# Kernel optimization log

Hardware: AMD Instinct MI355X
Metric: run time of the kernel (lower is better)

The kernel has to match this reference:

```python
import jax, jax.numpy as jnp
import numpy as np

V, BLK, H, D, L = 32000, 1024, 16, 1024, 3
HD = D // H  # 64
B, T = 4, 1024


def _layernorm(x, g, b, eps=1e-5):
    mu = jnp.mean(x, axis=-1, keepdims=True)
    var = jnp.mean(jnp.square(x - mu), axis=-1, keepdims=True)
    return (x - mu) * jax.lax.rsqrt(var + eps) * g + b


def setup_inputs() -> dict:
    key = jax.random.key(0)
    ks = jax.random.split(key, 32)
    s = 0.02
    inp = {}
    inp["idx"] = jax.random.randint(ks[0], (B, T), 0, V)
    inp["target"] = jax.random.randint(ks[1], (B, T), 0, V)
    inp["tok_emb"] = jax.random.normal(ks[2], (V, D), jnp.float32) * s
    inp["pos_emb"] = jax.random.normal(ks[3], (BLK, D), jnp.float32) * s
    inp["wq"] = jax.random.normal(ks[4], (L, H, D, HD), jnp.float32) * s
    inp["wk"] = jax.random.normal(ks[5], (L, H, D, HD), jnp.float32) * s
    inp["wv"] = jax.random.normal(ks[6], (L, H, D, HD), jnp.float32) * s
    inp["wproj"] = jax.random.normal(ks[7], (L, D, D), jnp.float32) * s
    inp["bproj"] = jnp.zeros((L, D), jnp.float32)
    inp["ln1_g"] = jnp.ones((L, D), jnp.float32)
    inp["ln1_b"] = jnp.zeros((L, D), jnp.float32)
    inp["ln2_g"] = jnp.ones((L, D), jnp.float32)
    inp["ln2_b"] = jnp.zeros((L, D), jnp.float32)
    inp["w1"] = jax.random.normal(ks[8], (L, D, 4 * D), jnp.float32) * s
    inp["b1"] = jnp.zeros((L, 4 * D), jnp.float32)
    inp["w2"] = jax.random.normal(ks[9], (L, 4 * D, D), jnp.float32) * s
    inp["b2"] = jnp.zeros((L, D), jnp.float32)
    inp["lnf_g"] = jnp.ones((D,), jnp.float32)
    inp["lnf_b"] = jnp.zeros((D,), jnp.float32)
    inp["wlm"] = jax.random.normal(ks[10], (D, V), jnp.float32) * s
    inp["blm"] = jnp.zeros((V,), jnp.float32)
    return inp


def reference(idx, target, tok_emb, pos_emb, wq, wk, wv, wproj, bproj,
              ln1_g, ln1_b, ln2_g, ln2_b, w1, b1, w2, b2,
              lnf_g, lnf_b, wlm, blm):
    Bb, Tt = idx.shape
    x = tok_emb[idx] + pos_emb[:Tt]  # [B,T,D]
    mask = jnp.tril(jnp.ones((Tt, Tt), dtype=bool))  # causal
    scale = D ** -0.5  # NOTE: source scales by n_embd**-0.5, not head_size**-0.5
    for l in range(L):
        xn = _layernorm(x, ln1_g[l], ln1_b[l])
        q = jnp.einsum('btd,hde->bhte', xn, wq[l])
        k = jnp.einsum('btd,hde->bhte', xn, wk[l])
        v = jnp.einsum('btd,hde->bhte', xn, wv[l])
        scores = jnp.einsum('bhte,bhse->bhts', q, k) * scale
        scores = jnp.where(mask, scores, -jnp.inf)
        attn = jax.nn.softmax(scores, axis=-1)
        o = jnp.einsum('bhts,bhse->bhte', attn, v)
        o = o.transpose(0, 2, 1, 3).reshape(Bb, Tt, D)  # concat heads
        x = x + o @ wproj[l] + bproj[l]
        xn2 = _layernorm(x, ln2_g[l], ln2_b[l])
        h = jax.nn.relu(xn2 @ w1[l] + b1[l])
        x = x + h @ w2[l] + b2[l]
    x = _layernorm(x, lnf_g, lnf_b)
    logits = x @ wlm + blm  # [B,T,V]
    logp = jax.nn.log_softmax(logits, axis=-1)
    nll = -jnp.take_along_axis(logp, target[..., None], axis=-1)[..., 0]
    loss = jnp.mean(nll)
    return logits, loss
```

## Files before the change

### kernel.cpp

```cpp
#include <hip/hip_runtime.h>
#include <math.h>

#define Dn   1024
#define Hn   16
#define HDn  64
#define Tn   1024
#define Bn   4
#define Vn   32000
#define Ln   3
#define NT   (Bn*Tn)

typedef __attribute__((ext_vector_type(8))) short bf16x8;
typedef __attribute__((ext_vector_type(4))) float f32x4;

__device__ __forceinline__ float b2f(unsigned short u) {
  union { float f; unsigned int i; } c; c.i = ((unsigned int)u) << 16; return c.f;
}
__device__ __forceinline__ unsigned short f2b(float f) {
  union { float f; unsigned int i; } c; c.f = f;
  unsigned int r = (c.i + 0x7FFFu + ((c.i >> 16) & 1u)) >> 16;
  return (unsigned short)r;
}

#define GLOAD_LDS16(g, l) __builtin_amdgcn_global_load_lds( \
    (const __attribute__((address_space(1))) void*)(g),     \
    (__attribute__((address_space(3))) void*)(l), 16, 0, 0)

#define SBAR()  __builtin_amdgcn_s_barrier()
#define SCHED() __builtin_amdgcn_sched_barrier(0)

__global__ __launch_bounds__(256) void embed_kernel(
    const int* __restrict__ idx, const float* __restrict__ tok,
    const float* __restrict__ pos, float* __restrict__ x) {
  int row = blockIdx.x;
  int t = row & (Tn - 1);
  int token = idx[row];
  const float4* tp = (const float4*)(tok + (size_t)token * Dn);
  const float4* pp = (const float4*)(pos + (size_t)t * Dn);
  float4* xp = (float4*)(x + (size_t)row * Dn);
  int i = threadIdx.x;
  float4 a = tp[i], b = pp[i];
  xp[i] = make_float4(a.x + b.x, a.y + b.y, a.z + b.z, a.w + b.w);
}

__global__ __launch_bounds__(256) void ln_kernel(
    const float* __restrict__ x, const float* __restrict__ g,
    const float* __restrict__ b, unsigned short* __restrict__ y) {
  int row = blockIdx.x;
  const float4* xr = (const float4*)(x + (size_t)row * Dn);
  __shared__ float red[4];
  int lane = threadIdx.x & 63, w = threadIdx.x >> 6;

  float4 v = xr[threadIdx.x];
  float s = v.x + v.y + v.z + v.w;
  #pragma unroll
  for (int o = 32; o > 0; o >>= 1) s += __shfl_down(s, o, 64);
  if (lane == 0) red[w] = s;
  __syncthreads();
  float mu = (red[0] + red[1] + red[2] + red[3]) * (1.0f / Dn);
  __syncthreads();

  float dx = v.x - mu, dy = v.y - mu, dz = v.z - mu, dw = v.w - mu;
  float ss = dx*dx + dy*dy + dz*dz + dw*dw;
  #pragma unroll
  for (int o = 32; o > 0; o >>= 1) ss += __shfl_down(ss, o, 64);
  if (lane == 0) red[w] = ss;
  __syncthreads();
  float var = (red[0] + red[1] + red[2] + red[3]) * (1.0f / Dn);
  float inv = rsqrtf(var + 1e-5f);

  float4 gv = ((const float4*)g)[threadIdx.x];
  float4 bv = ((const float4*)b)[threadIdx.x];
  ushort4 o4;
  o4.x = f2b(dx*inv*gv.x + bv.x);
  o4.y = f2b(dy*inv*gv.y + bv.y);
  o4.z = f2b(dz*inv*gv.z + bv.z);
  o4.w = f2b(dw*inv*gv.w + bv.w);
  ((ushort4*)(y + (size_t)row * Dn))[threadIdx.x] = o4;
}

__global__ __launch_bounds__(256) void wcast_kernel(
    const float* __restrict__ src, unsigned short* __restrict__ dst,
    int K, int M, long long bsk, long long bsh) {
  __shared__ float t[32][33];
  int m0 = blockIdx.x << 5, k0 = blockIdx.y << 5;
  int tid = threadIdx.x;
  int ml = tid & 31, kl = tid >> 5;
  #pragma unroll
  for (int p = 0; p < 4; ++p) {
    int k = k0 + kl + p * 8;
    int m = m0 + ml;
    t[ml][kl + p * 8] = src[(size_t)k * bsk + (size_t)(m >> 6) * bsh + (m & 63)];
  }
  __syncthreads();
  int kl2 = tid & 31, ml2 = tid >> 5;
  #pragma unroll
  for (int p = 0; p < 4; ++p) {
    int m = m0 + ml2 + p * 8;
    int k = k0 + kl2;
    dst[(size_t)m * K + k] = f2b(t[ml2 + p * 8][kl2]);
  }
}

__global__ __launch_bounds__(256) void wcast3_kernel(
    const float* __restrict__ s0, const float* __restrict__ s1,
    const float* __restrict__ s2, unsigned short* __restrict__ dst) {
  const float* src = (blockIdx.z == 0) ? s0 : (blockIdx.z == 1) ? s1 : s2;
  unsigned short* d = dst + (size_t)blockIdx.z * 1024 * Dn;
  __shared__ float t[32][33];
  int m0 = blockIdx.x << 5, k0 = blockIdx.y << 5;
  int tid = threadIdx.x;
  int ml = tid & 31, kl = tid >> 5;
  #pragma unroll
  for (int p = 0; p < 4; ++p) {
    int k = k0 + kl + p * 8;
    int m = m0 + ml;
    t[ml][kl + p * 8] = src[(size_t)k * HDn + (size_t)(m >> 6) * (Dn * HDn) + (m & 63)];
  }
  __syncthreads();
  int kl2 = tid & 31, ml2 = tid >> 5;
  #pragma unroll
  for (int p = 0; p < 4; ++p) {
    int m = m0 + ml2 + p * 8;
    int k = k0 + kl2;
    d[(size_t)m * Dn + k] = f2b(t[ml2 + p * 8][kl2]);
  }
}

__global__ __launch_bounds__(512) void mm_bf16(
    const unsigned short* __restrict__ A, const unsigned short* __restrict__ BT,
    const float* __restrict__ bias, const float* __restrict__ res,
    float* __restrict__ Cf, unsigned short* __restrict__ Ch,
    int N, int K, int M, int relu) {
  __shared__ __align__(16) unsigned short As[3][128 * 32];
  __shared__ __align__(16) unsigned short Bs[3][128 * 32];
  const int tid = threadIdx.x;
  const int lane = tid & 63, w = tid >> 6, g = lane >> 4;
  const int wr = w >> 2, wc = w & 3;
  const int n0 = blockIdx.x << 7, m0 = blockIdx.y << 7;

  f32x4 acc[4][2];
  #pragma unroll
  for (int i = 0; i < 4; ++i)
    #pragma unroll
    for (int j = 0; j < 2; ++j)
      acc[i][j] = (f32x4){0.f, 0.f, 0.f, 0.f};

  const int srow = tid >> 2, su = tid & 3;
  const int sks = su ^ ((srow >> 1) & 3);
  const unsigned short* a_g = A + (size_t)(n0 + srow) * K + sks * 8;
  const unsigned short* b_g = BT + (size_t)(m0 + srow) * K + sks * 8;

  int a_off[4], b_off[2];
  #pragma unroll
  for (int f = 0; f < 4; ++f) {
    int row = wr * 64 + f * 16 + (lane & 15);
    a_off[f] = row * 64 + ((g ^ ((row >> 1) & 3)) << 4);
  }
  #pragma unroll
  for (int f = 0; f < 2; ++f) {
    int col = wc * 32 + f * 16 + (lane & 15);
    b_off[f] = col * 64 + ((g ^ ((col >> 1) & 3)) << 4);
  }

#define MM_STAGE(buf, kk) do {                                   \
    GLOAD_LDS16(a_g + (kk), As[buf] + tid * 8);                  \
    GLOAD_LDS16(b_g + (kk), Bs[buf] + tid * 8); } while (0)

#define MM_COMPUTE(buf) do {                                     \
    bf16x8 af[4], bfr[2];                                        \
    _Pragma("unroll")                                            \
    for (int f = 0; f < 4; ++f)                                  \
      af[f] = *(const bf16x8*)((const char*)As[buf] + a_off[f]); \
    _Pragma("unroll")                                            \
    for (int f = 0; f < 2; ++f)                                  \
      bfr[f] = *(const bf16x8*)((const char*)Bs[buf] + b_off[f]);\
    _Pragma("unroll")                                            \
    for (int i = 0; i < 4; ++i)                                  \
      _Pragma("unroll")                                          \
      for (int j = 0; j < 2; ++j)                                \
        acc[i][j] = __builtin_amdgcn_mfma_f32_16x16x32_bf16(af[i], bfr[j], acc[i][j], 0, 0, 0); } while (0)

  MM_STAGE(0, 0);
  MM_STAGE(1, 32);
  int bc = 0, bp = 2;
  for (int k0 = 0; k0 < K; k0 += 32) {
    if (k0 + 32 < K) asm volatile("s_waitcnt vmcnt(2)" ::: "memory");
    else             asm volatile("s_waitcnt vmcnt(0)" ::: "memory");
    SCHED(); SBAR(); SCHED();
    if (k0 + 64 < K) MM_STAGE(bp, k0 + 64);
    MM_COMPUTE(bc);
    bc = (bc == 2) ? 0 : bc + 1;
    bp = (bp == 2) ? 0 : bp + 1;
  }

  #pragma unroll
  for (int fc = 0; fc < 2; ++fc) {
    int colg = m0 + wc * 32 + fc * 16 + (lane & 15);
    float bz = bias ? bias[colg] : 0.f;
    #pragma unroll
    for (int fr = 0; fr < 4; ++fr) {
      #pragma unroll
      for (int i = 0; i < 4; ++i) {
        int rowg = n0 + wr * 64 + fr * 16 + (g << 2) + i;
        float v = acc[fr][fc][i] + bz;
        if (res) v += res[(size_t)rowg * M + colg];
        if (relu) v = fmaxf(v, 0.f);
        if (Cf) Cf[(size_t)rowg * M + colg] = v;
        else    Ch[(size_t)rowg * M + colg] = f2b(v);
      }
    }
  }
#undef MM_STAGE
#undef MM_COMPUTE
}

template<int OMODE>
__global__ __launch_bounds__(512) void mm512_bf16(
    const unsigned short* __restrict__ A, const unsigned short* __restrict__ BT,
    const float* __restrict__ bias, const float* __restrict__ res,
    float* __restrict__ Cf, unsigned short* __restrict__ Ch,
    float* __restrict__ rowsum, int N, int K, int M, int relu) {
  __shared__ __align__(16) unsigned short As[3][128 * 32];
  __shared__ __align__(16) unsigned short Bs[3][256 * 32];
  __shared__ float rsum2[OMODE == 4 ? 128 * 4 : 4];
  const int tid = threadIdx.x;
  const int lane = tid & 63, w = tid >> 6, g = lane >> 4;
  const int wr = w >> 2, wc = w & 3;
  const int n0 = blockIdx.x << 7, m0 = blockIdx.y << 8;

  f32x4 acc[4][4];
  #pragma unroll
  for (int i = 0; i < 4; ++i)
    #pragma unroll
    for (int j = 0; j < 4; ++j)
      acc[i][j] = (f32x4){0.f, 0.f, 0.f, 0.f};

  const int arow = tid >> 2, au = tid & 3;
  const int aks = au ^ ((arow >> 1) & 3);
  const unsigned short* a_g = A + (size_t)(n0 + arow) * K + aks * 8;
  const int brow1 = (tid + 512) >> 2;
  const int bks0 = au ^ ((arow >> 1) & 3);
  const int bks1 = au ^ ((brow1 >> 1) & 3);
  const unsigned short* b_g0 = BT + (size_t)(m0 + arow) * K + bks0 * 8;
  const unsigned short* b_g1 = BT + (size_t)(m0 + brow1) * K + bks1 * 8;

  int a_off[4], b_off[4];
  #pragma unroll
  for (int f = 0; f < 4; ++f) {
    int row = wr * 64 + f * 16 + (lane & 15);
    a_off[f] = row * 64 + ((g ^ ((row >> 1) & 3)) << 4);
    int col = wc * 64 + f * 16 + (lane & 15);
    b_off[f] = col * 64 + ((g ^ ((col >> 1) & 3)) << 4);
  }

#define MM5_STAGE(buf, kk) do {                                  \
    GLOAD_LDS16(a_g + (kk), As[buf] + tid * 8);                  \
    GLOAD_LDS16(b_g0 + (kk), Bs[buf] + tid * 8);                 \
    GLOAD_LDS16(b_g1 + (kk), Bs[buf] + (tid + 512) * 8); } while (0)

#define MM5_COMPUTE(buf) do {                                    \
    bf16x8 af[4], bfr[4];                                        \
    _Pragma("unroll")                                            \
    for (int f = 0; f < 4; ++f) {                                \
      af[f]  = *(const bf16x8*)((const char*)As[buf] + a_off[f]);\
      bfr[f] = *(const bf16x8*)((const char*)Bs[buf] + b_off[f]);\
    }                                                            \
    _Pragma("unroll")                                            \
    for (int i = 0; i < 4; ++i)                                  \
      _Pragma("unroll")                                          \
      for (int j = 0; j < 4; ++j)                                \
        acc[i][j] = __builtin_amdgcn_mfma_f32_16x16x32_bf16(af[i], bfr[j], acc[i][j], 0, 0, 0); } while (0)

  MM5_STAGE(0, 0);
  MM5_STAGE(1, 32);
  int bc = 0, bp = 2;
  for (int k0 = 0; k0 < K; k0 += 32) {
    if (k0 + 32 < K) asm volatile("s_waitcnt vmcnt(3)" ::: "memory");
    else             asm volatile("s_waitcnt vmcnt(0)" ::: "memory");
    SCHED(); SBAR(); SCHED();
    if (k0 + 64 < K) MM5_STAGE(bp, k0 + 64);
    MM5_COMPUTE(bc);
    bc = (bc == 2) ? 0 : bc + 1;
    bp = (bp == 2) ? 0 : bp + 1;
  }

  if (OMODE == 0) {
    #pragma unroll
    for (int fc = 0; fc < 4; ++fc) {
      int colg = m0 + wc * 64 + fc * 16 + (lane & 15);
      float bz = bias ? bias[colg] : 0.f;
      #pragma unroll
      for (int fr = 0; fr < 4; ++fr) {
        #pragma unroll
        for (int i = 0; i < 4; ++i) {
          int rowg = n0 + wr * 64 + fr * 16 + (g << 2) + i;
          float v = acc[fr][fc][i] + bz;
          if (res) v += res[(size_t)rowg * M + colg];
          if (relu) v = fmaxf(v, 0.f);
          if (Cf) Cf[(size_t)rowg * M + colg] = v;
          else    Ch[(size_t)rowg * M + colg] = f2b(v);
        }
      }
    }
  } else if (OMODE == 3) {
    unsigned short* kb  = Ch + (size_t)NT * Dn;
    unsigned short* vtb = Ch + 2 * (size_t)NT * Dn;
    #pragma unroll
    for (int fc = 0; fc < 4; ++fc) {
      int colg = m0 + wc * 64 + fc * 16 + (lane & 15);
      int sel = colg >> 10, hh = (colg >> 6) & 15, e = colg & 63;
      #pragma unroll
      for (int fr = 0; fr < 4; ++fr) {
        int rowg0 = n0 + wr * 64 + fr * 16 + (g << 2);
        int b = rowg0 >> 10, t0 = rowg0 & 1023;
        if (sel == 2) {
          ushort4 pk;
          pk.x = f2b(acc[fr][fc][0]); pk.y = f2b(acc[fr][fc][1]);
          pk.z = f2b(acc[fr][fc][2]); pk.w = f2b(acc[fr][fc][3]);
          *(ushort4*)&vtb[(((size_t)(b * 16 + hh) * 64) + e) * 1024 + t0] = pk;
        } else {
          unsigned short* dst = (sel == 0) ? Ch : kb;
          #pragma unroll
          for (int i = 0; i < 4; ++i)
            dst[(((size_t)(b * 16 + hh) * 1024) + t0 + i) * 64 + e] = f2b(acc[fr][fc][i]);
        }
      }
    }
  } else {
    #pragma unroll
    for (int fr = 0; fr < 4; ++fr) {
      #pragma unroll
      for (int i = 0; i < 4; ++i) {
        int rloc = wr * 64 + fr * 16 + (g << 2) + i;
        int rowg = n0 + rloc;
        float es = 0.f;
        #pragma unroll
        for (int fc = 0; fc < 4; ++fc) {
          int colg = m0 + wc * 64 + fc * 16 + (lane & 15);
          float v = acc[fr][fc][i] + bias[colg];
          __builtin_nontemporal_store(v, &Cf[(size_t)rowg * M + colg]);
          es += __expf(v);
        }
        es += __shfl_xor(es, 1); es += __shfl_xor(es, 2);
        es += __shfl_xor(es, 4); es += __shfl_xor(es, 8);
        if ((lane & 15) == 0) rsum2[rloc * 4 + wc] = es;
      }
    }
    __syncthreads();
    if (tid < 128)
      atomicAdd(&rowsum[n0 + tid],
                rsum2[tid * 4 + 0] + rsum2[tid * 4 + 1] +
                rsum2[tid * 4 + 2] + rsum2[tid * 4 + 3]);
  }
#undef MM5_STAGE
#undef MM5_COMPUTE
}

__global__ __launch_bounds__(256) void fattn_kernel(
    const unsigned short* __restrict__ qg, const unsigned short* __restrict__ kg,
    const unsigned short* __restrict__ vtg, unsigned short* __restrict__ ob) {
  const int bid = blockIdx.x;
  const int qt = bid & 15, bh = bid >> 4;
  const int b = bh >> 4, h = bh & 15;
  const int tid = threadIdx.x, lane = tid & 63, w = tid >> 6, g = lane >> 4;

  __shared__ __align__(16) unsigned short Ks[2][64 * 64];
  __shared__ __align__(16) unsigned short Vs[2][64 * 64];
  __shared__ __align__(16) unsigned short Pb[4][16 * 64];

  const unsigned short* kbase = kg + (size_t)bh * Tn * HDn;
  const unsigned short* vbase = vtg + (size_t)bh * HDn * Tn;

  const int qrow = qt * 64 + w * 16 + (lane & 15);
  const unsigned short* qptr = qg + ((size_t)bh * Tn + qrow) * HDn;
  bf16x8 qf0 = *(const bf16x8*)(qptr + g * 8);
  bf16x8 qf1 = *(const bf16x8*)(qptr + 32 + g * 8);

  f32x4 accO[4];
  #pragma unroll
  for (int dt = 0; dt < 4; ++dt) accO[dt] = (f32x4){0.f, 0.f, 0.f, 0.f};
  float mrun[4] = {-1e30f, -1e30f, -1e30f, -1e30f};
  float lrun[4] = {0.f, 0.f, 0.f, 0.f};

  const float scale = 0.03125f;
  const int qout0 = qt * 64 + w * 16 + 4 * g;

  unsigned short* pb = &Pb[w][0];
  const int nsteps = qt + 1;

#define FA_STAGE(buf, s0_) do {                                              \
    _Pragma("unroll")                                                        \
    for (int r = 0; r < 2; ++r) {                                            \
      int c = tid + 256 * r;                                                 \
      int srow = c >> 3, u = c & 7;                                          \
      GLOAD_LDS16(kbase + (size_t)((s0_) + srow) * HDn + ((u ^ (srow & 7)) * 8), Ks[buf] + c * 8); \
    }                                                                        \
    _Pragma("unroll")                                                        \
    for (int r = 0; r < 2; ++r) {                                            \
      int c = tid + 256 * r;                                                 \
      int d = c >> 3, u = c & 7;                                             \
      GLOAD_LDS16(vbase + (size_t)d * Tn + (s0_) + ((u ^ (d & 7)) * 8), Vs[buf] + c * 8); \
    } } while (0)

  FA_STAGE(0, 0);
  int cur = 0;

  for (int st = 0; st < nsteps; ++st) {
    const int s0 = st * 64;
    if (st + 1 < nsteps) {
      FA_STAGE(cur ^ 1, s0 + 64);
      asm volatile("s_waitcnt vmcnt(4)" ::: "memory");
    } else {
      asm volatile("s_waitcnt vmcnt(0)" ::: "memory");
    }
    SCHED(); SBAR(); SCHED();

    float p[4][4];
    #pragma unroll
    for (int sub = 0; sub < 4; ++sub) {
      int srow = sub * 16 + (lane & 15);
      const char* kr = (const char*)Ks[cur] + srow * 128;
      bf16x8 kf0 = *(const bf16x8*)(kr + ((g ^ (srow & 7)) * 16));
      bf16x8 kf1 = *(const bf16x8*)(kr + (((4 + g) ^ (srow & 7)) * 16));
      f32x4 s4 = (f32x4){0.f, 0.f, 0.f, 0.f};
      s4 = __builtin_amdgcn_mfma_f32_16x16x32_bf16(qf0, kf0, s4, 0, 0, 0);
      s4 = __builtin_amdgcn_mfma_f32_16x16x32_bf16(qf1, kf1, s4, 0, 0, 0);
      int sg = s0 + srow;
      #pragma unroll
      for (int i = 0; i < 4; ++i)
        p[sub][i] = (sg > qout0 + i) ? -1e30f : s4[i] * scale;
    }

    #pragma unroll
    for (int i = 0; i < 4; ++i) {
      float v = fmaxf(fmaxf(p[0][i], p[1][i]), fmaxf(p[2][i], p[3][i]));
      v = fmaxf(v, __shfl_xor(v, 1)); v = fmaxf(v, __shfl_xor(v, 2));
      v = fmaxf(v, __shfl_xor(v, 4)); v = fmaxf(v, __shfl_xor(v, 8));
      float nm = fmaxf(mrun[i], v);
      float fac = __expf(mrun[i] - nm);
      mrun[i] = nm;
      #pragma unroll
      for (int dt = 0; dt < 4; ++dt) accO[dt][i] *= fac;
      float sum = 0.f;
      #pragma unroll
      for (int sub = 0; sub < 4; ++sub) {
        float e = __expf(p[sub][i] - nm);
        p[sub][i] = e;
        sum += e;
      }
      sum += __shfl_xor(sum, 1); sum += __shfl_xor(sum, 2);
      sum += __shfl_xor(sum, 4); sum += __shfl_xor(sum, 8);
      lrun[i] = lrun[i] * fac + sum;
    }

    #pragma unroll
    for (int sub = 0; sub < 4; ++sub) {
      int s = sub * 16 + (lane & 15);
      #pragma unroll
      for (int i = 0; i < 4; ++i) {
        int q = 4 * g + i;
        pb[q * 64 + (((s >> 3) ^ (q & 7)) * 8) + (s & 7)] = f2b(p[sub][i]);
      }
    }

    #pragma unroll
    for (int sc = 0; sc < 2; ++sc) {
      int qq = lane & 15;
      bf16x8 pa = *(const bf16x8*)((const char*)pb + qq * 128 + (((sc * 4 + g) ^ (qq & 7)) * 16));
      #pragma unroll
      for (int dt = 0; dt < 4; ++dt) {
        int d = dt * 16 + (lane & 15);
        bf16x8 vf = *(const bf16x8*)((const char*)Vs[cur] + d * 128 + (((sc * 4 + g) ^ (d & 7)) * 16));
        accO[dt] = __builtin_amdgcn_mfma_f32_16x16x32_bf16(pa, vf, accO[dt], 0, 0, 0);
      }
    }

    SCHED(); SBAR(); SCHED();
    cur ^= 1;
  }
#undef FA_STAGE

  float rinv[4];
  #pragma unroll
  for (int i = 0; i < 4; ++i) rinv[i] = 1.0f / lrun[i];
  #pragma unroll
  for (int dt = 0; dt < 4; ++dt) {
    int dcol = h * 64 + dt * 16 + (lane & 15);
    #pragma unroll
    for (int i = 0; i < 4; ++i) {
      int t = qout0 + i;
      ob[((size_t)(b * Tn + t)) * Dn + dcol] = f2b(accO[dt][i] * rinv[i]);
    }
  }
}

__global__ __launch_bounds__(256) void loss_kernel(
    const float* __restrict__ logits, const float* __restrict__ rowsum,
    const int* __restrict__ target, float* __restrict__ out_loss) {
  __shared__ float red[4];
  int lane = threadIdx.x & 63, w = threadIdx.x >> 6;
  float s = 0.f;
  for (int row = threadIdx.x; row < NT; row += 256) {
    float lt = logits[(size_t)row * Vn + target[row]];
    s += logf(rowsum[row]) - lt;
  }
  #pragma unroll
  for (int off = 32; off > 0; off >>= 1) s += __shfl_down(s, off, 64);
  if (lane == 0) red[w] = s;
  __syncthreads();
  if (threadIdx.x == 0)
    *out_loss = (red[0] + red[1] + red[2] + red[3]) * (1.0f / NT);
}

static inline void launch_wcast(const float* src, unsigned short* dst, int K, int M,
                                long long bsk, long long bsh, hipStream_t s) {
  dim3 g(M >> 5, K >> 5);
  wcast_kernel<<<g, 256, 0, s>>>(src, dst, K, M, bsk, bsh);
}

static inline void launch_mm(const unsigned short* A, const unsigned short* BT,
                             const float* bias, const float* res,
                             float* Cf, unsigned short* Ch,
                             int N, int K, int M, int relu, hipStream_t s) {
  dim3 g(N >> 7, M >> 7);
  mm_bf16<<<g, 512, 0, s>>>(A, BT, bias, res, Cf, Ch, N, K, M, relu);
}

template<int OMODE>
static inline void launch_mm512(const unsigned short* A, const unsigned short* BT,
                                const float* bias, const float* res,
                                float* Cf, unsigned short* Ch, float* rowsum,
                                int N, int K, int M, int relu, hipStream_t s) {
  dim3 g(N >> 7, M >> 8);
  mm512_bf16<OMODE><<<g, 512, 0, s>>>(A, BT, bias, res, Cf, Ch, rowsum, N, K, M, relu);
}

extern "C" void kernel_launch(void* const* d_in, const int* in_sizes, int n_in,
                              void* d_out, int out_size, void* d_ws, size_t ws_size,
                              hipStream_t stream) {
  const int*   idx    = (const int*)d_in[0];
  const int*   target = (const int*)d_in[1];
  const float* tok    = (const float*)d_in[2];
  const float* pos    = (const float*)d_in[3];
  const float* wq     = (const float*)d_in[4];
  const float* wk     = (const float*)d_in[5];
  const float* wv     = (const float*)d_in[6];
  const float* wproj  = (const float*)d_in[7];
  const float* bproj  = (const float*)d_in[8];
  const float* ln1g   = (const float*)d_in[9];
  const float* ln1b   = (const float*)d_in[10];
  const float* ln2g   = (const float*)d_in[11];
  const float* ln2b   = (const float*)d_in[12];
  const float* w1     = (const float*)d_in[13];
  const float* b1     = (const float*)d_in[14];
  const float* w2     = (const float*)d_in[15];
  const float* b2     = (const float*)d_in[16];
  const float* lnfg   = (const float*)d_in[17];
  const float* lnfb   = (const float*)d_in[18];
  const float* wlm    = (const float*)d_in[19];
  const float* blm    = (const float*)d_in[20];

  float* out = (float*)d_out;

  char* p = (char*)d_ws;
  float* x  = (float*)p;                 p += (size_t)NT * Dn * 4;
  unsigned short* xn = (unsigned short*)p; p += (size_t)NT * Dn * 2;
  unsigned short* reg = (unsigned short*)p; p += (size_t)NT * 4 * Dn * 2;
  unsigned short* wT = (unsigned short*)p; p += (size_t)Vn * Dn * 2;
  float* rowsum = (float*)p;

  unsigned short* qb  = reg;
  unsigned short* kb  = reg + (size_t)NT * Dn;
  unsigned short* vtb = reg + 2 * (size_t)NT * Dn;
  unsigned short* ob  = reg + 3 * (size_t)NT * Dn;
  unsigned short* hb  = reg;

  embed_kernel<<<NT, 256, 0, stream>>>(idx, tok, pos, x);

  for (int l = 0; l < Ln; ++l) {
    const float* wq_l = wq + (size_t)l * Hn * Dn * HDn;
    const float* wk_l = wk + (size_t)l * Hn * Dn * HDn;
    const float* wv_l = wv + (size_t)l * Hn * Dn * HDn;

    ln_kernel<<<NT, 256, 0, stream>>>(x, ln1g + l * Dn, ln1b + l * Dn, xn);

    {
      dim3 g3(32, 32, 3);
      wcast3_kernel<<<g3, 256, 0, stream>>>(wq_l, wk_l, wv_l, wT);
    }
    launch_mm512<3>(xn, wT, nullptr, nullptr, nullptr, qb, nullptr, NT, Dn, 3072, 0, stream);

    fattn_kernel<<<Bn * Hn * (Tn / 64), 256, 0, stream>>>(qb, kb, vtb, ob);

    launch_wcast(wproj + (size_t)l * Dn * Dn, wT, Dn, Dn, Dn, 64, stream);
    launch_mm(ob, wT, bproj + l * Dn, x, x, nullptr, NT, Dn, Dn, 0, stream);

    ln_kernel<<<NT, 256, 0, stream>>>(x, ln2g + l * Dn, ln2b + l * Dn, xn);

    launch_wcast(w1 + (size_t)l * Dn * 4 * Dn, wT, Dn, 4 * Dn, 4 * Dn, 64, stream);
    launch_mm512<0>(xn, wT, b1 + l * 4 * Dn, nullptr, nullptr, hb, nullptr, NT, Dn, 4 * Dn, 1, stream);
    launch_wcast(w2 + (size_t)l * 4 * Dn * Dn, wT, 4 * Dn, Dn, Dn, 64, stream);
    launch_mm(hb, wT, b2 + l * Dn, x, x, nullptr, NT, 4 * Dn, Dn, 0, stream);
  }

  ln_kernel<<<NT, 256, 0, stream>>>(x, lnfg, lnfb, xn);

  hipMemsetAsync(rowsum, 0, NT * sizeof(float), stream);
  launch_wcast(wlm, wT, Dn, Vn, Vn, 64, stream);
  launch_mm512<4>(xn, wT, blm, nullptr, out, nullptr, rowsum, NT, Dn, Vn, 0, stream);

  loss_kernel<<<1, 256, 0, stream>>>(out, rowsum, target, out + (size_t)NT * Vn);
}
```

Measured before the change: 1.207 ms.

## Enlarge wide GEMM tiles to 256x256 with K=64 stages and XCD-aware block swizzle

The wide GEMM kernel used for QKV, FFN-up and LM-head moves from 128x256 output tiles with a triple-buffered K=32 pipeline to 256x256 tiles. Each 256x256 tile uses a double-buffered K=64 pipeline with an XOR-swizzled LDS layout, and each wave holds 8x4 MFMA accumulators. This raises arithmetic intensity per byte loaded and halves the number of blocks. A block-index remap groups consecutive tiles onto the same XCD, applied to both GEMM kernels, to improve L2 locality. In exchange the kernel uses about 128KB of LDS, so only one block fits per CU, and the end-of-iteration full vmcnt(0) wait limits overlap of loads with compute.

```diff
diff --git a/kernel.cpp b/kernel.cpp
--- a/kernel.cpp
+++ b/kernel.cpp
@@ -28,6 +28,13 @@
 
 #define SBAR()  __builtin_amdgcn_s_barrier()
 #define SCHED() __builtin_amdgcn_sched_barrier(0)
+
+__device__ __forceinline__ void xcd_swz(int& bx, int& by) {
+  int gx = gridDim.x, nwg = gx * gridDim.y;
+  int lin = by * gx + bx;
+  int swz = (lin & 7) * (nwg >> 3) + (lin >> 3);
+  bx = swz % gx; by = swz / gx;
+}
 
 __global__ __launch_bounds__(256) void embed_kernel(
     const int* __restrict__ idx, const float* __restrict__ tok,
@@ -137,7 +144,9 @@
   const int tid = threadIdx.x;
   const int lane = tid & 63, w = tid >> 6, g = lane >> 4;
   const int wr = w >> 2, wc = w & 3;
-  const int n0 = blockIdx.x << 7, m0 = blockIdx.y << 7;
+  int bx = blockIdx.x, by = blockIdx.y;
+  xcd_swz(bx, by);
+  const int n0 = bx << 7, m0 = by << 7;
 
   f32x4 acc[4][2];
   #pragma unroll
@@ -216,73 +225,113 @@
 }
 
 template<int OMODE>
-__global__ __launch_bounds__(512) void mm512_bf16(
+__global__ __launch_bounds__(512, 2) void mm256_bf16(
     const unsigned short* __restrict__ A, const unsigned short* __restrict__ BT,
     const float* __restrict__ bias, const float* __restrict__ res,
     float* __restrict__ Cf, unsigned short* __restrict__ Ch,
     float* __restrict__ rowsum, int N, int K, int M, int relu) {
-  __shared__ __align__(16) unsigned short As[3][128 * 32];
-  __shared__ __align__(16) unsigned short Bs[3][256 * 32];
-  __shared__ float rsum2[OMODE == 4 ? 128 * 4 : 4];
+  __shared__ __align__(16) unsigned short As[2][256 * 64];
+  __shared__ __align__(16) unsigned short Bs[2][256 * 64];
+  __shared__ float rsum2[OMODE == 4 ? 256 * 4 : 4];
   const int tid = threadIdx.x;
   const int lane = tid & 63, w = tid >> 6, g = lane >> 4;
   const int wr = w >> 2, wc = w & 3;
-  const int n0 = blockIdx.x << 7, m0 = blockIdx.y << 8;
-
-  f32x4 acc[4][4];
-  #pragma unroll
-  for (int i = 0; i < 4; ++i)
+  int bx = blockIdx.x, by = blockIdx.y;
+  xcd_swz(bx, by);
+  const int n0 = bx << 8, m0 = by << 8;
+
+  f32x4 acc[8][4];
+  #pragma unroll
+  for (int i = 0; i < 8; ++i)
     #pragma unroll
     for (int j = 0; j < 4; ++j)
       acc[i][j] = (f32x4){0.f, 0.f, 0.f, 0.f};
 
-  const int arow = tid >> 2, au = tid & 3;
-  const int aks = au ^ ((arow >> 1) & 3);
-  const unsigned short* a_g = A + (size_t)(n0 + arow) * K + aks * 8;
-  const int brow1 = (tid + 512) >> 2;
-  const int bks0 = au ^ ((arow >> 1) & 3);
-  const int bks1 = au ^ ((brow1 >> 1) & 3);
-  const unsigned short* b_g0 = BT + (size_t)(m0 + arow) * K + bks0 * 8;
-  const unsigned short* b_g1 = BT + (size_t)(m0 + brow1) * K + bks1 * 8;
-
-  int a_off[4], b_off[4];
-  #pragma unroll
-  for (int f = 0; f < 4; ++f) {
-    int row = wr * 64 + f * 16 + (lane & 15);
-    a_off[f] = row * 64 + ((g ^ ((row >> 1) & 3)) << 4);
-    int col = wc * 64 + f * 16 + (lane & 15);
-    b_off[f] = col * 64 + ((g ^ ((col >> 1) & 3)) << 4);
-  }
-
-#define MM5_STAGE(buf, kk) do {                                  \
-    GLOAD_LDS16(a_g + (kk), As[buf] + tid * 8);                  \
-    GLOAD_LDS16(b_g0 + (kk), Bs[buf] + tid * 8);                 \
-    GLOAD_LDS16(b_g1 + (kk), Bs[buf] + (tid + 512) * 8); } while (0)
-
-#define MM5_COMPUTE(buf) do {                                    \
-    bf16x8 af[4], bfr[4];                                        \
-    _Pragma("unroll")                                            \
-    for (int f = 0; f < 4; ++f) {                                \
-      af[f]  = *(const bf16x8*)((const char*)As[buf] + a_off[f]);\
-      bfr[f] = *(const bf16x8*)((const char*)Bs[buf] + b_off[f]);\
-    }                                                            \
-    _Pragma("unroll")                                            \
-    for (int i = 0; i < 4; ++i)                                  \
-      _Pragma("unroll")                                          \
-      for (int j = 0; j < 4; ++j)                                \
-        acc[i][j] = __builtin_amdgcn_mfma_f32_16x16x32_bf16(af[i], bfr[j], acc[i][j], 0, 0, 0); } while (0)
-
-  MM5_STAGE(0, 0);
-  MM5_STAGE(1, 32);
-  int bc = 0, bp = 2;
-  for (int k0 = 0; k0 < K; k0 += 32) {
-    if (k0 + 32 < K) asm volatile("s_waitcnt vmcnt(3)" ::: "memory");
-    else             asm volatile("s_waitcnt vmcnt(0)" ::: "memory");
+  const unsigned short* ag[4];
+  const unsigned short* bg[4];
+  int lofs[4];
+  #pragma unroll
+  for (int j = 0; j < 4; ++j) {
+    int c = tid + 512 * j;
+    int row = c >> 3, u = c & 7;
+    int ks = u ^ (row & 7);
+    ag[j] = A + (size_t)(n0 + row) * K + ks * 8;
+    bg[j] = BT + (size_t)(m0 + row) * K + ks * 8;
+    lofs[j] = c * 8;
+  }
+
+  int aoff[2][2][4], boff[2][2][2];
+  #pragma unroll
+  for (int h0 = 0; h0 < 2; ++h0)
+    #pragma unroll
+    for (int ks = 0; ks < 2; ++ks) {
+      #pragma unroll
+      for (int fr = 0; fr < 4; ++fr) {
+        int r = wr * 128 + h0 * 64 + fr * 16 + (lane & 15);
+        aoff[h0][ks][fr] = r * 128 + (((g + ks * 4) ^ (r & 7)) << 4);
+      }
+      #pragma unroll
+      for (int fb = 0; fb < 2; ++fb) {
+        int cB = wc * 64 + ks * 32 + fb * 16 + (lane & 15);
+        (void)cB;
+      }
+    }
+  #pragma unroll
+  for (int h1 = 0; h1 < 2; ++h1)
+    #pragma unroll
+    for (int ks = 0; ks < 2; ++ks)
+      #pragma unroll
+      for (int fb = 0; fb < 2; ++fb) {
+        int cB = wc * 64 + h1 * 32 + fb * 16 + (lane & 15);
+        boff[h1][ks][fb] = cB * 128 + (((g + ks * 4) ^ (cB & 7)) << 4);
+      }
+
+  #pragma unroll
+  for (int j = 0; j < 4; ++j) {
+    GLOAD_LDS16(ag[j], As[0] + lofs[j]);
+    GLOAD_LDS16(bg[j], Bs[0] + lofs[j]);
+  }
+  asm volatile("s_waitcnt vmcnt(0)" ::: "memory");
+  SCHED(); SBAR(); SCHED();
+
+  int cur = 0;
+  const int NKT = K >> 6;
+  for (int kt = 0; kt < NKT; ++kt) {
+    if (kt + 1 < NKT) {
+      const int kn = (kt + 1) << 6;
+      #pragma unroll
+      for (int j = 0; j < 4; ++j) {
+        GLOAD_LDS16(ag[j] + kn, As[cur ^ 1] + lofs[j]);
+        GLOAD_LDS16(bg[j] + kn, Bs[cur ^ 1] + lofs[j]);
+      }
+    }
+    const char* Ab = (const char*)As[cur];
+    const char* Bb = (const char*)Bs[cur];
+    #pragma unroll
+    for (int h0 = 0; h0 < 2; ++h0) {
+      #pragma unroll
+      for (int ks = 0; ks < 2; ++ks) {
+        bf16x8 af[4];
+        #pragma unroll
+        for (int fr = 0; fr < 4; ++fr)
+          af[fr] = *(const bf16x8*)(Ab + aoff[h0][ks][fr]);
+        #pragma unroll
+        for (int h1 = 0; h1 < 2; ++h1) {
+          bf16x8 b0 = *(const bf16x8*)(Bb + boff[h1][ks][0]);
+          bf16x8 b1 = *(const bf16x8*)(Bb + boff[h1][ks][1]);
+          #pragma unroll
+          for (int fr = 0; fr < 4; ++fr) {
+            acc[h0 * 4 + fr][h1 * 2 + 0] =
+                __builtin_amdgcn_mfma_f32_16x16x32_bf16(af[fr], b0, acc[h0 * 4 + fr][h1 * 2 + 0], 0, 0, 0);
+            acc[h0 * 4 + fr][h1 * 2 + 1] =
+                __builtin_amdgcn_mfma_f32_16x16x32_bf16(af[fr], b1, acc[h0 * 4 + fr][h1 * 2 + 1], 0, 0, 0);
+          }
+        }
+      }
+    }
+    asm volatile("s_waitcnt vmcnt(0)" ::: "memory");
     SCHED(); SBAR(); SCHED();
-    if (k0 + 64 < K) MM5_STAGE(bp, k0 + 64);
-    MM5_COMPUTE(bc);
-    bc = (bc == 2) ? 0 : bc + 1;
-    bp = (bp == 2) ? 0 : bp + 1;
+    cur ^= 1;
   }
 
   if (OMODE == 0) {
@@ -291,10 +340,10 @@
       int colg = m0 + wc * 64 + fc * 16 + (lane & 15);
       float bz = bias ? bias[colg] : 0.f;
       #pragma unroll
-      for (int fr = 0; fr < 4; ++fr) {
+      for (int fr = 0; fr < 8; ++fr) {
         #pragma unroll
         for (int i = 0; i < 4; ++i) {
-          int rowg = n0 + wr * 64 + fr * 16 + (g << 2) + i;
+          int rowg = n0 + wr * 128 + fr * 16 + (g << 2) + i;
           float v = acc[fr][fc][i] + bz;
           if (res) v += res[(size_t)rowg * M + colg];
           if (relu) v = fmaxf(v, 0.f);
@@ -311,8 +360,8 @@
       int colg = m0 + wc * 64 + fc * 16 + (lane & 15);
       int sel = colg >> 10, hh = (colg >> 6) & 15, e = colg & 63;
       #pragma unroll
-      for (int fr = 0; fr < 4; ++fr) {
-        int rowg0 = n0 + wr * 64 + fr * 16 + (g << 2);
+      for (int fr = 0; fr < 8; ++fr) {
+        int rowg0 = n0 + wr * 128 + fr * 16 + (g << 2);
         int b = rowg0 >> 10, t0 = rowg0 & 1023;
         if (sel == 2) {
           ushort4 pk;
@@ -329,10 +378,10 @@
     }
   } else {
     #pragma unroll
-    for (int fr = 0; fr < 4; ++fr) {
+    for (int fr = 0; fr < 8; ++fr) {
       #pragma unroll
       for (int i = 0; i < 4; ++i) {
-        int rloc = wr * 64 + fr * 16 + (g << 2) + i;
+        int rloc = wr * 128 + fr * 16 + (g << 2) + i;
         int rowg = n0 + rloc;
         float es = 0.f;
         #pragma unroll
@@ -348,13 +397,11 @@
       }
     }
     __syncthreads();
-    if (tid < 128)
+    if (tid < 256)
       atomicAdd(&rowsum[n0 + tid],
                 rsum2[tid * 4 + 0] + rsum2[tid * 4 + 1] +
                 rsum2[tid * 4 + 2] + rsum2[tid * 4 + 3]);
   }
-#undef MM5_STAGE
-#undef MM5_COMPUTE
 }
 
 __global__ __launch_bounds__(256) void fattn_kernel(
@@ -528,12 +575,12 @@
 }
 
 template<int OMODE>
-static inline void launch_mm512(const unsigned short* A, const unsigned short* BT,
+static inline void launch_mm256(const unsigned short* A, const unsigned short* BT,
                                 const float* bias, const float* res,
                                 float* Cf, unsigned short* Ch, float* rowsum,
                                 int N, int K, int M, int relu, hipStream_t s) {
-  dim3 g(N >> 7, M >> 8);
-  mm512_bf16<OMODE><<<g, 512, 0, s>>>(A, BT, bias, res, Cf, Ch, rowsum, N, K, M, relu);
+  dim3 g(N >> 8, M >> 8);
+  mm256_bf16<OMODE><<<g, 512, 0, s>>>(A, BT, bias, res, Cf, Ch, rowsum, N, K, M, relu);
 }
 
 extern "C" void kernel_launch(void* const* d_in, const int* in_sizes, int n_in,
@@ -589,7 +636,7 @@
       dim3 g3(32, 32, 3);
       wcast3_kernel<<<g3, 256, 0, stream>>>(wq_l, wk_l, wv_l, wT);
     }
-    launch_mm512<3>(xn, wT, nullptr, nullptr, nullptr, qb, nullptr, NT, Dn, 3072, 0, stream);
+    launch_mm256<3>(xn, wT, nullptr, nullptr, nullptr, qb, nullptr, NT, Dn, 3072, 0, stream);
 
     fattn_kernel<<<Bn * Hn * (Tn / 64), 256, 0, stream>>>(qb, kb, vtb, ob);
 
@@ -599,7 +646,7 @@
     ln_kernel<<<NT, 256, 0, stream>>>(x, ln2g + l * Dn, ln2b + l * Dn, xn);
 
     launch_wcast(w1 + (size_t)l * Dn * 4 * Dn, wT, Dn, 4 * Dn, 4 * Dn, 64, stream);
-    launch_mm512<0>(xn, wT, b1 + l * 4 * Dn, nullptr, nullptr, hb, nullptr, NT, Dn, 4 * Dn, 1, stream);
+    launch_mm256<0>(xn, wT, b1 + l * 4 * Dn, nullptr, nullptr, hb, nullptr, NT, Dn, 4 * Dn, 1, stream);
     launch_wcast(w2 + (size_t)l * 4 * Dn * Dn, wT, 4 * Dn, Dn, Dn, 64, stream);
     launch_mm(hb, wT, b2 + l * Dn, x, x, nullptr, NT, 4 * Dn, Dn, 0, stream);
   }
@@ -608,7 +655,7 @@
 
   hipMemsetAsync(rowsum, 0, NT * sizeof(float), stream);
   launch_wcast(wlm, wT, Dn, Vn, Vn, 64, stream);
-  launch_mm512<4>(xn, wT, blm, nullptr, out, nullptr, rowsum, NT, Dn, Vn, 0, stream);
+  launch_mm256<4>(xn, wT, blm, nullptr, out, nullptr, rowsum, NT, Dn, Vn, 0, stream);
 
   loss_kernel<<<1, 256, 0, stream>>>(out, rowsum, target, out + (size_t)NT * Vn);
 }
```

Measured after the change: 1.279 ms. +5.9%, slower.
